# Kernel optimization log

Measured on AMD Instinct MI355X. Metric: run time of the kernel, lower is better.

The kernel has to match this reference:

```python
import jax, jax.numpy as jnp
import numpy as np

NUM_EXPERTS = 32
TOP_K = 4
HIDDEN = 2048
INTER = 768


def setup_inputs() -> dict:
    key = jax.random.key(0)
    k1, k2, k3, k4 = jax.random.split(key, 4)
    hidden_states = jax.random.normal(k1, (4, 512, HIDDEN), dtype=jnp.float32)
    gate = jax.random.normal(k2, (HIDDEN, NUM_EXPERTS), dtype=jnp.float32) * 0.02
    gate_up_proj = jax.random.normal(k3, (NUM_EXPERTS, HIDDEN, 2 * INTER), dtype=jnp.float32) * 0.02
    down_proj = jax.random.normal(k4, (NUM_EXPERTS, INTER, HIDDEN), dtype=jnp.float32) * 0.02
    return {"hidden_states": hidden_states, "gate": gate,
            "gate_up_proj": gate_up_proj, "down_proj": down_proj}


def reference(hidden_states, gate, gate_up_proj, down_proj):
    batch_size = hidden_states.shape[0]
    x = hidden_states.reshape(-1, HIDDEN)  # (T, D)
    num_tokens = x.shape[0]

    # Router
    router_logits = jnp.einsum('TD,DE->TE', x, gate)
    routing_weights = jax.nn.softmax(router_logits.astype(jnp.float32), axis=-1)
    top_k_weights, top_k_indices = jax.lax.top_k(routing_weights, TOP_K)
    top_k_weights = top_k_weights / top_k_weights.sum(axis=-1, keepdims=True)
    top_k_weights = top_k_weights.astype(x.dtype)

    # Scatter top-k weights into full (T, E) matrix
    router_weights = jnp.zeros((num_tokens, NUM_EXPERTS), dtype=x.dtype)
    token_indices = jnp.broadcast_to(jnp.arange(num_tokens)[:, None], top_k_indices.shape)
    router_weights = router_weights.at[token_indices, top_k_indices].set(top_k_weights)

    # Dense all-expert experts pass (faithful to original: computes every expert per token)
    gate_up = jnp.einsum('TD,EDF->TEF', x, gate_up_proj)  # (T, E, 2F)
    g, u = jnp.split(gate_up, 2, axis=-1)
    gated = u * jax.nn.silu(g)  # (T, E, F)
    next_states = jnp.einsum('TEF,EFD->TED', gated, down_proj)
    next_states = (next_states * router_weights[..., None]).sum(axis=1)  # (T, D)
    return next_states.reshape(batch_size, -1, HIDDEN)
```

## Files before the change

kernel.cpp:

```cpp
#include <hip/hip_runtime.h>

#define T_TOKENS 2048
#define HIDDEN   2048
#define NEXPERT  32
#define TOPK     4
#define INTER    768
#define GUF      (2*INTER)
#define NPAIRS   (T_TOKENS*TOPK)
#define BM       128
#define BK       32
#define MT_MAX   95
#define NT1      6
#define NT2      8
#define NK1      (HIDDEN/BK)
#define NK2      (INTER/BK)

typedef short  bh8 __attribute__((ext_vector_type(8)));
typedef float  fx4 __attribute__((ext_vector_type(4)));

#define AS1 __attribute__((address_space(1)))
#define AS3 __attribute__((address_space(3)))

__device__ __forceinline__ void gload_lds16(const void* g, const void* lds_generic){
    __builtin_amdgcn_global_load_lds(
        (const AS1 void*)(unsigned long long)g,
        (AS3 void*)(unsigned int)(unsigned long long)lds_generic,
        16, 0, 0);
}

__device__ __forceinline__ unsigned int pack2bf(float a, float b){
    unsigned ua = __float_as_uint(a) + 0x8000u;
    unsigned ub = __float_as_uint(b) + 0x8000u;
    return __builtin_amdgcn_perm(ub, ua, 0x07060302u);
}
__device__ __forceinline__ unsigned short f2bfu(float f){
    return (unsigned short)((__float_as_uint(f) + 0x8000u) >> 16);
}
__device__ __forceinline__ float bf2f(unsigned short s){
    return __uint_as_float(((unsigned)s)<<16);
}

__global__ void cvt_x_k(const float* __restrict__ x, unsigned short* __restrict__ xb){
    int i = (blockIdx.x*256 + threadIdx.x)*8;
    float4 a = *(const float4*)(x+i);
    float4 b = *(const float4*)(x+i+4);
    uint4 o;
    o.x = pack2bf(a.x,a.y); o.y = pack2bf(a.z,a.w);
    o.z = pack2bf(b.x,b.y); o.w = pack2bf(b.z,b.w);
    *(uint4*)(xb+i) = o;
}

__global__ void router_k(const float* __restrict__ x, const float* __restrict__ gate,
                         int* __restrict__ topk_id, float* __restrict__ topk_w,
                         int* __restrict__ counts){
    const int t = blockIdx.x;
    const int l = threadIdx.x;
    const float* xr = x + (size_t)t*HIDDEN;
    float acc[NEXPERT];
#pragma unroll
    for (int e=0;e<NEXPERT;e++) acc[e]=0.f;
    for (int d=l; d<HIDDEN; d+=64){
        float xv = xr[d];
        const float4* g4 = (const float4*)(gate + (size_t)d*NEXPERT);
#pragma unroll
        for (int i=0;i<8;i++){
            float4 g = g4[i];
            acc[i*4+0] += xv*g.x; acc[i*4+1] += xv*g.y;
            acc[i*4+2] += xv*g.z; acc[i*4+3] += xv*g.w;
        }
    }
#pragma unroll
    for (int e=0;e<NEXPERT;e++){
#pragma unroll
        for (int m=1;m<64;m<<=1) acc[e] += __shfl_xor(acc[e], m, 64);
    }
    int ids[TOPK]; float lv[TOPK];
#pragma unroll
    for (int k=0;k<TOPK;k++){
        float m=-1e30f; int mi=0;
#pragma unroll
        for (int e=0;e<NEXPERT;e++){ if (acc[e]>m){ m=acc[e]; mi=e; } }
        ids[k]=mi; lv[k]=m; acc[mi]=-1e30f;
    }
    float ex[TOPK]; float s=0.f;
#pragma unroll
    for (int k=0;k<TOPK;k++){ ex[k]=__expf(lv[k]-lv[0]); s+=ex[k]; }
    if (l==0){
        float inv = 1.f/s;
#pragma unroll
        for (int k=0;k<TOPK;k++){
            topk_id[t*TOPK+k]=ids[k];
            topk_w[t*TOPK+k]=ex[k]*inv;
            atomicAdd(&counts[ids[k]],1);
        }
    }
}

__global__ void sched_k(const int* __restrict__ counts, int* __restrict__ offs,
                        int* __restrict__ cursors, int* __restrict__ nmt,
                        int* __restrict__ te, int* __restrict__ tr0, int* __restrict__ trn){
    if (threadIdx.x==0 && blockIdx.x==0){
        int tot=0, nm=0;
        for (int e=0;e<NEXPERT;e++){
            int c = counts[e];
            offs[e]=tot; cursors[e]=tot;
            for (int s=0;s<c;s+=BM){
                te[nm]=e; tr0[nm]=tot+s; trn[nm]=(c-s)<BM?(c-s):BM; nm++;
            }
            tot+=c;
        }
        *nmt = nm;
    }
}

__global__ void scatter_k(const int* __restrict__ topk_id, const float* __restrict__ topk_w,
                          int* __restrict__ cursors, int* __restrict__ pair_tok,
                          float* __restrict__ pair_w){
    int g = blockIdx.x*256 + threadIdx.x;
    int e = topk_id[g];
    float w = topk_w[g];
    int pos = atomicAdd(&cursors[e],1);
    pair_tok[pos] = g>>2;
    pair_w[pos]  = w;
}

#define TILE_DECODE()                                              \
    const int nwg = gridDim.x;                                     \
    const int q = nwg>>3, r = nwg&7;                               \
    const int xcd = blockIdx.x & 7, bidx = blockIdx.x >> 3;        \
    const int L = (xcd<r ? xcd*(q+1) : r*(q+1)+(xcd-r)*q) + bidx;  \
    const int mt = L % MT_MAX, nt = L / MT_MAX;                    \
    if (mt >= *nmt) return;                                        \
    const int e = te[mt], row0 = tr0[mt], rows = trn[mt];

__global__ __launch_bounds__(512,4) void gemm1_k(
        const unsigned short* __restrict__ xb, const float* __restrict__ gup,
        const int* __restrict__ nmt, const int* __restrict__ te,
        const int* __restrict__ tr0, const int* __restrict__ trn,
        const int* __restrict__ pair_tok,
        unsigned short* __restrict__ gu){
    __shared__ __align__(16) unsigned short As[2][BM*32];
    __shared__ __align__(16) unsigned short Bs[2][256*40];
    __shared__ int s_tok[BM];

    TILE_DECODE()
    const int n0 = nt*256;

    const int t = threadIdx.x;
    if (t < BM){
        int p = row0 + t; if (p > NPAIRS-1) p = NPAIRS-1;
        s_tok[t] = pair_tok[p];
    }
    __syncthreads();

    const int w = t>>6, lane = t&63;
    const int l15 = lane & 15, kb = lane >> 4;
    const int wr = w & 3, wc = w >> 2;
    const int sA = (l15>>1)&3;

    const int arow = w*16 + (lane>>2);
    const int ck0 = (lane&3) ^ ((lane>>3)&3);
    const unsigned short* asrc = xb + (size_t)s_tok[arow]*HIDDEN + ck0*8;

    const int cp = t & 127, kh = t >> 7;
    const float* bsrc = gup + (size_t)e*HIDDEN*GUF + (size_t)kh*8*GUF + (n0 + 2*cp);
    const unsigned wb0 = (unsigned)((2*cp)*80 + ((kh ^ (cp&3))<<4));

    fx4 acc[2][8];
#pragma unroll
    for (int i=0;i<2;i++)
#pragma unroll
        for (int j=0;j<8;j++) acc[i][j] = (fx4)0.f;

    float2 f0,f1,f2,f3,f4,f5,f6,f7;

#define LOADB1(KS) do{ const float* _bp = bsrc + (size_t)(KS)*BK*GUF;           \
    f0=*(const float2*)(_bp);        f1=*(const float2*)(_bp+GUF);              \
    f2=*(const float2*)(_bp+2*GUF);  f3=*(const float2*)(_bp+3*GUF);            \
    f4=*(const float2*)(_bp+4*GUF);  f5=*(const float2*)(_bp+5*GUF);            \
    f6=*(const float2*)(_bp+6*GUF);  f7=*(const float2*)(_bp+7*GUF); }while(0)

#define WRITEB(BUF) do{ char* _bb = (char*)Bs[BUF];                             \
    uint4 _c0, _c1;                                                             \
    _c0.x=pack2bf(f0.x,f1.x); _c0.y=pack2bf(f2.x,f3.x);                         \
    _c0.z=pack2bf(f4.x,f5.x); _c0.w=pack2bf(f6.x,f7.x);                         \
    _c1.x=pack2bf(f0.y,f1.y); _c1.y=pack2bf(f2.y,f3.y);                         \
    _c1.z=pack2bf(f4.y,f5.y); _c1.w=pack2bf(f6.y,f7.y);                         \
    *(uint4*)(_bb + wb0) = _c0; *(uint4*)(_bb + wb0 + 80) = _c1; }while(0)

#define STAGEA1(KS,BUF) gload_lds16(asrc + (KS)*BK, &As[BUF][(w*16)*32])

#define COMPUTE(BUF) do{                                                        \
    const unsigned short* _Ak = As[BUF];                                        \
    const char* _Bb = (const char*)Bs[BUF];                                     \
    bh8 _a0 = *(const bh8*)(_Ak + (wr*32+l15)*32    + ((kb^sA)<<3));            \
    bh8 _a1 = *(const bh8*)(_Ak + (wr*32+16+l15)*32 + ((kb^sA)<<3));            \
    _Pragma("unroll")                                                           \
    for (int c=0;c<8;c++){                                                      \
        bh8 _b = *(const bh8*)(_Bb + (wc*128 + c*16 + l15)*80 + ((kb^sA)<<4));  \
        acc[0][c] = __builtin_amdgcn_mfma_f32_16x16x32_bf16(_a0,_b,acc[0][c],0,0,0); \
        acc[1][c] = __builtin_amdgcn_mfma_f32_16x16x32_bf16(_a1,_b,acc[1][c],0,0,0); \
    } }while(0)

    STAGEA1(0,0); LOADB1(0);
    __syncthreads();
    WRITEB(0);
    __syncthreads();

    for (int k=0;k<NK1;k++){
        const int kn = k+1;
        if (kn < NK1){ LOADB1(kn); STAGEA1(kn, kn&1); }
        COMPUTE(k&1);
        __syncthreads();
        if (kn < NK1) WRITEB(kn&1);
        __syncthreads();
    }

    const int rbase = wr*32 + kb*4;
#pragma unroll
    for (int mr=0;mr<2;mr++){
#pragma unroll
        for (int qq=0;qq<4;qq++){
            int row = rbase + mr*16 + qq;
            if (row < rows){
                size_t prow = (size_t)(row0 + row)*GUF + n0 + wc*128 + l15;
#pragma unroll
                for (int c=0;c<8;c++)
                    gu[prow + c*16] = f2bfu(acc[mr][c][qq]);
            }
        }
    }
#undef LOADB1
#undef STAGEA1
}

__global__ void silu_k(const unsigned short* __restrict__ gu,
                       const float* __restrict__ pair_w,
                       unsigned short* __restrict__ gated){
    const int t = threadIdx.x;
    const int r = (t >= 96) ? 1 : 0;
    const int jg = t - r*96;
    const int p = blockIdx.x*2 + r;
    bh8 g8 = *(const bh8*)(gu + (size_t)p*GUF + jg*8);
    bh8 u8 = *(const bh8*)(gu + (size_t)p*GUF + INTER + jg*8);
    float wgt = pair_w[p];
    bh8 o;
#pragma unroll
    for (int j=0;j<8;j++){
        float g = bf2f((unsigned short)g8[j]);
        float u = bf2f((unsigned short)u8[j]);
        float sil = g / (1.f + __expf(-g));
        o[j] = (short)f2bfu(sil*u*wgt);
    }
    *(bh8*)(gated + (size_t)p*INTER + jg*8) = o;
}

__global__ __launch_bounds__(512,4) void gemm2_k(
        const unsigned short* __restrict__ gated, const float* __restrict__ down,
        const int* __restrict__ nmt, const int* __restrict__ te,
        const int* __restrict__ tr0, const int* __restrict__ trn,
        const int* __restrict__ pair_tok, float* __restrict__ out){
    __shared__ __align__(16) unsigned short As[2][BM*32];
    __shared__ __align__(16) unsigned short Bs[2][256*40];
    __shared__ int s_tok[BM];

    TILE_DECODE()
    const int n0 = nt*256;

    const int t = threadIdx.x;
    if (t < BM){
        int p = row0 + t; if (p > NPAIRS-1) p = NPAIRS-1;
        s_tok[t] = pair_tok[p];
    }
    __syncthreads();

    const int w = t>>6, lane = t&63;
    const int l15 = lane & 15, kb = lane >> 4;
    const int wr = w & 3, wc = w >> 2;
    const int sA = (l15>>1)&3;

    const int arow = w*16 + (lane>>2);
    const int ck0 = (lane&3) ^ ((lane>>3)&3);
    int ap = row0 + arow; if (ap > NPAIRS-1) ap = NPAIRS-1;
    const unsigned short* asrc = gated + (size_t)ap*INTER + ck0*8;

    const int cp = t & 127, kh = t >> 7;
    const float* bsrc = down + (size_t)e*INTER*HIDDEN + (size_t)kh*8*HIDDEN + (n0 + 2*cp);
    const unsigned wb0 = (unsigned)((2*cp)*80 + ((kh ^ (cp&3))<<4));

    fx4 acc[2][8];
#pragma unroll
    for (int i=0;i<2;i++)
#pragma unroll
        for (int j=0;j<8;j++) acc[i][j] = (fx4)0.f;

    float2 f0,f1,f2,f3,f4,f5,f6,f7;

#define LOADB2(KS) do{ const float* _bp = bsrc + (size_t)(KS)*BK*HIDDEN;        \
    f0=*(const float2*)(_bp);           f1=*(const float2*)(_bp+HIDDEN);        \
    f2=*(const float2*)(_bp+2*HIDDEN);  f3=*(const float2*)(_bp+3*HIDDEN);      \
    f4=*(const float2*)(_bp+4*HIDDEN);  f5=*(const float2*)(_bp+5*HIDDEN);      \
    f6=*(const float2*)(_bp+6*HIDDEN);  f7=*(const float2*)(_bp+7*HIDDEN); }while(0)

#define STAGEA2(KS,BUF) gload_lds16(asrc + (KS)*BK, &As[BUF][(w*16)*32])

    STAGEA2(0,0); LOADB2(0);
    __syncthreads();
    WRITEB(0);
    __syncthreads();

    for (int k=0;k<NK2;k++){
        const int kn = k+1;
        if (kn < NK2){ LOADB2(kn); STAGEA2(kn, kn&1); }
        COMPUTE(k&1);
        __syncthreads();
        if (kn < NK2) WRITEB(kn&1);
        __syncthreads();
    }

    const int rbase = wr*32 + kb*4;
#pragma unroll
    for (int mr=0;mr<2;mr++){
#pragma unroll
        for (int qq=0;qq<4;qq++){
            int row = rbase + mr*16 + qq;
            if (row < rows){
                float* orow = out + (size_t)s_tok[row]*HIDDEN + n0 + wc*128 + l15;
#pragma unroll
                for (int c=0;c<8;c++)
                    atomicAdd(orow + c*16, acc[mr][c][qq]);
            }
        }
    }
}

extern "C" void kernel_launch(void* const* d_in, const int* in_sizes, int n_in,
                              void* d_out, int out_size, void* d_ws, size_t ws_size,
                              hipStream_t stream){
    const float* x    = (const float*)d_in[0];
    const float* gate = (const float*)d_in[1];
    const float* gup  = (const float*)d_in[2];
    const float* down = (const float*)d_in[3];
    float* out = (float*)d_out;
    char*  ws  = (char*)d_ws;

    int*   topk_id  = (int*)  (ws + 0x00000);
    float* topk_w   = (float*)(ws + 0x08000);
    int*   counts   = (int*)  (ws + 0x10000);
    int*   cursors  = (int*)  (ws + 0x10080);
    int*   offs     = (int*)  (ws + 0x10100);
    int*   nmt      = (int*)  (ws + 0x10180);
    int*   te       = (int*)  (ws + 0x10200);
    int*   tr0      = (int*)  (ws + 0x10400);
    int*   trn      = (int*)  (ws + 0x10600);
    int*   pair_tok = (int*)  (ws + 0x10800);
    float* pair_w   = (float*)(ws + 0x18800);
    unsigned short* gated = (unsigned short*)(ws + 0x21000);
    unsigned short* xb    = (unsigned short*)(ws + 0xC60000);
    unsigned short* gu    = (unsigned short*)(ws + 0x1460000);

    hipMemsetAsync(d_out, 0, (size_t)out_size*sizeof(float), stream);
    hipMemsetAsync(counts, 0, NEXPERT*sizeof(int), stream);

    cvt_x_k  <<<T_TOKENS*HIDDEN/(256*8), 256, 0, stream>>>(x, xb);
    router_k <<<T_TOKENS, 64, 0, stream>>>(x, gate, topk_id, topk_w, counts);
    sched_k  <<<1, 64, 0, stream>>>(counts, offs, cursors, nmt, te, tr0, trn);
    scatter_k<<<NPAIRS/256, 256, 0, stream>>>(topk_id, topk_w, cursors, pair_tok, pair_w);
    gemm1_k  <<<MT_MAX*NT1, 512, 0, stream>>>(xb, gup, nmt, te, tr0, trn, pair_tok, gu);
    silu_k   <<<NPAIRS/2, 192, 0, stream>>>(gu, pair_w, gated);
    gemm2_k  <<<MT_MAX*NT2, 512, 0, stream>>>(gated, down, nmt, te, tr0, trn, pair_tok, out);
}
```

Baseline: 510.9 us.

## Enlarge expert GEMM M-tile to 256 rows with 1024-thread blocks

Doubles the row tile of both grouped expert GEMMs from 128 to 256 pairs and uses 1024 threads per block, so each B weight tile (converted from fp32 to bf16 on the fly) is reused across more rows. The B-loading scheme changes to float4 loads with a new swizzled LDS write, each wave computes 64x64 instead of 32x128, and tile decode becomes m-major so adjacent blocks share the same A rows. Larger tiles mean more padding waste for small experts, fewer blocks, and higher register pressure under the launch bounds.

```diff
diff --git a/kernel.cpp b/kernel.cpp
--- a/kernel.cpp
+++ b/kernel.cpp
@@ -7,9 +7,9 @@
 #define INTER    768
 #define GUF      (2*INTER)
 #define NPAIRS   (T_TOKENS*TOPK)
-#define BM       128
+#define BM       256
 #define BK       32
-#define MT_MAX   95
+#define MT_MAX   63
 #define NT1      6
 #define NT2      8
 #define NK1      (HIDDEN/BK)
@@ -124,16 +124,41 @@
     pair_w[pos]  = w;
 }
 
-#define TILE_DECODE()                                              \
+#define TILE_DECODE(NTC)                                           \
     const int nwg = gridDim.x;                                     \
     const int q = nwg>>3, r = nwg&7;                               \
     const int xcd = blockIdx.x & 7, bidx = blockIdx.x >> 3;        \
     const int L = (xcd<r ? xcd*(q+1) : r*(q+1)+(xcd-r)*q) + bidx;  \
-    const int mt = L % MT_MAX, nt = L / MT_MAX;                    \
+    const int mt = L / (NTC), nt = L % (NTC);                      \
     if (mt >= *nmt) return;                                        \
     const int e = te[mt], row0 = tr0[mt], rows = trn[mt];
 
-__global__ __launch_bounds__(512,4) void gemm1_k(
+#define MFMA16(A,B,C) __builtin_amdgcn_mfma_f32_16x16x32_bf16(A,B,C,0,0,0)
+
+#define COMPUTE(BUF) do{                                                        \
+    const unsigned short* _Ak = As[BUF];                                        \
+    const char* _Bb = (const char*)Bs[BUF];                                     \
+    bh8 _a0 = *(const bh8*)(_Ak + (wr*64      + l15)*32 + ((kb^sA)<<3));        \
+    bh8 _a1 = *(const bh8*)(_Ak + (wr*64 + 16 + l15)*32 + ((kb^sA)<<3));        \
+    bh8 _a2 = *(const bh8*)(_Ak + (wr*64 + 32 + l15)*32 + ((kb^sA)<<3));        \
+    bh8 _a3 = *(const bh8*)(_Ak + (wr*64 + 48 + l15)*32 + ((kb^sA)<<3));        \
+    _Pragma("unroll")                                                           \
+    for (int c=0;c<4;c++){                                                      \
+        const int bc = wc*64 + c*16 + l15;                                      \
+        bh8 _b = *(const bh8*)(_Bb + bc*80 + ((kb ^ ((bc>>3)&3))<<4));          \
+        acc[0][c] = MFMA16(_a0,_b,acc[0][c]);                                   \
+        acc[1][c] = MFMA16(_a1,_b,acc[1][c]);                                   \
+        acc[2][c] = MFMA16(_a2,_b,acc[2][c]);                                   \
+        acc[3][c] = MFMA16(_a3,_b,acc[3][c]);                                   \
+    } }while(0)
+
+#define WRITEB(BUF) do{ char* _bb = (char*)Bs[BUF];                             \
+    *(unsigned*)(_bb + wb      ) = pack2bf(rv0.x, rv1.x);                       \
+    *(unsigned*)(_bb + wb +  80) = pack2bf(rv0.y, rv1.y);                       \
+    *(unsigned*)(_bb + wb + 160) = pack2bf(rv0.z, rv1.z);                       \
+    *(unsigned*)(_bb + wb + 240) = pack2bf(rv0.w, rv1.w); }while(0)
+
+__global__ __launch_bounds__(1024,4) void gemm1_k(
         const unsigned short* __restrict__ xb, const float* __restrict__ gup,
         const int* __restrict__ nmt, const int* __restrict__ te,
         const int* __restrict__ tr0, const int* __restrict__ trn,
@@ -143,7 +168,7 @@
     __shared__ __align__(16) unsigned short Bs[2][256*40];
     __shared__ int s_tok[BM];
 
-    TILE_DECODE()
+    TILE_DECODE(NT1)
     const int n0 = nt*256;
 
     const int t = threadIdx.x;
@@ -162,45 +187,22 @@
     const int ck0 = (lane&3) ^ ((lane>>3)&3);
     const unsigned short* asrc = xb + (size_t)s_tok[arow]*HIDDEN + ck0*8;
 
-    const int cp = t & 127, kh = t >> 7;
-    const float* bsrc = gup + (size_t)e*HIDDEN*GUF + (size_t)kh*8*GUF + (n0 + 2*cp);
-    const unsigned wb0 = (unsigned)((2*cp)*80 + ((kh ^ (cp&3))<<4));
-
-    fx4 acc[2][8];
-#pragma unroll
-    for (int i=0;i<2;i++)
-#pragma unroll
-        for (int j=0;j<8;j++) acc[i][j] = (fx4)0.f;
-
-    float2 f0,f1,f2,f3,f4,f5,f6,f7;
-
+    const int tlow = t & 63, th = t >> 6;
+    const int col4 = tlow*4, bd0 = th*2;
+    const int gq = (tlow>>1)&3;
+    const unsigned wb = (unsigned)(col4*80 + (((bd0>>3) ^ gq)<<4) + (bd0&7)*2);
+    const float* bsrc = gup + (size_t)e*HIDDEN*GUF + (size_t)bd0*GUF + (n0 + col4);
+
+    fx4 acc[4][4];
+#pragma unroll
+    for (int i=0;i<4;i++)
+#pragma unroll
+        for (int j=0;j<4;j++) acc[i][j] = (fx4)0.f;
+
+    float4 rv0, rv1;
 #define LOADB1(KS) do{ const float* _bp = bsrc + (size_t)(KS)*BK*GUF;           \
-    f0=*(const float2*)(_bp);        f1=*(const float2*)(_bp+GUF);              \
-    f2=*(const float2*)(_bp+2*GUF);  f3=*(const float2*)(_bp+3*GUF);            \
-    f4=*(const float2*)(_bp+4*GUF);  f5=*(const float2*)(_bp+5*GUF);            \
-    f6=*(const float2*)(_bp+6*GUF);  f7=*(const float2*)(_bp+7*GUF); }while(0)
-
-#define WRITEB(BUF) do{ char* _bb = (char*)Bs[BUF];                             \
-    uint4 _c0, _c1;                                                             \
-    _c0.x=pack2bf(f0.x,f1.x); _c0.y=pack2bf(f2.x,f3.x);                         \
-    _c0.z=pack2bf(f4.x,f5.x); _c0.w=pack2bf(f6.x,f7.x);                         \
-    _c1.x=pack2bf(f0.y,f1.y); _c1.y=pack2bf(f2.y,f3.y);                         \
-    _c1.z=pack2bf(f4.y,f5.y); _c1.w=pack2bf(f6.y,f7.y);                         \
-    *(uint4*)(_bb + wb0) = _c0; *(uint4*)(_bb + wb0 + 80) = _c1; }while(0)
-
+    rv0 = *(const float4*)(_bp); rv1 = *(const float4*)(_bp + GUF); }while(0)
 #define STAGEA1(KS,BUF) gload_lds16(asrc + (KS)*BK, &As[BUF][(w*16)*32])
-
-#define COMPUTE(BUF) do{                                                        \
-    const unsigned short* _Ak = As[BUF];                                        \
-    const char* _Bb = (const char*)Bs[BUF];                                     \
-    bh8 _a0 = *(const bh8*)(_Ak + (wr*32+l15)*32    + ((kb^sA)<<3));            \
-    bh8 _a1 = *(const bh8*)(_Ak + (wr*32+16+l15)*32 + ((kb^sA)<<3));            \
-    _Pragma("unroll")                                                           \
-    for (int c=0;c<8;c++){                                                      \
-        bh8 _b = *(const bh8*)(_Bb + (wc*128 + c*16 + l15)*80 + ((kb^sA)<<4));  \
-        acc[0][c] = __builtin_amdgcn_mfma_f32_16x16x32_bf16(_a0,_b,acc[0][c],0,0,0); \
-        acc[1][c] = __builtin_amdgcn_mfma_f32_16x16x32_bf16(_a1,_b,acc[1][c],0,0,0); \
-    } }while(0)
 
     STAGEA1(0,0); LOADB1(0);
     __syncthreads();
@@ -216,16 +218,15 @@
         __syncthreads();
     }
 
-    const int rbase = wr*32 + kb*4;
-#pragma unroll
-    for (int mr=0;mr<2;mr++){
+#pragma unroll
+    for (int mr=0;mr<4;mr++){
 #pragma unroll
         for (int qq=0;qq<4;qq++){
-            int row = rbase + mr*16 + qq;
+            int row = wr*64 + mr*16 + kb*4 + qq;
             if (row < rows){
-                size_t prow = (size_t)(row0 + row)*GUF + n0 + wc*128 + l15;
-#pragma unroll
-                for (int c=0;c<8;c++)
+                size_t prow = (size_t)(row0 + row)*GUF + n0 + wc*64 + l15;
+#pragma unroll
+                for (int c=0;c<4;c++)
                     gu[prow + c*16] = f2bfu(acc[mr][c][qq]);
             }
         }
@@ -255,7 +256,7 @@
     *(bh8*)(gated + (size_t)p*INTER + jg*8) = o;
 }
 
-__global__ __launch_bounds__(512,4) void gemm2_k(
+__global__ __launch_bounds__(1024,4) void gemm2_k(
         const unsigned short* __restrict__ gated, const float* __restrict__ down,
         const int* __restrict__ nmt, const int* __restrict__ te,
         const int* __restrict__ tr0, const int* __restrict__ trn,
@@ -264,7 +265,7 @@
     __shared__ __align__(16) unsigned short Bs[2][256*40];
     __shared__ int s_tok[BM];
 
-    TILE_DECODE()
+    TILE_DECODE(NT2)
     const int n0 = nt*256;
 
     const int t = threadIdx.x;
@@ -284,24 +285,21 @@
     int ap = row0 + arow; if (ap > NPAIRS-1) ap = NPAIRS-1;
     const unsigned short* asrc = gated + (size_t)ap*INTER + ck0*8;
 
-    const int cp = t & 127, kh = t >> 7;
-    const float* bsrc = down + (size_t)e*INTER*HIDDEN + (size_t)kh*8*HIDDEN + (n0 + 2*cp);
-    const unsigned wb0 = (unsigned)((2*cp)*80 + ((kh ^ (cp&3))<<4));
-
-    fx4 acc[2][8];
-#pragma unroll
-    for (int i=0;i<2;i++)
-#pragma unroll
-        for (int j=0;j<8;j++) acc[i][j] = (fx4)0.f;
-
-    float2 f0,f1,f2,f3,f4,f5,f6,f7;
-
+    const int tlow = t & 63, th = t >> 6;
+    const int col4 = tlow*4, bd0 = th*2;
+    const int gq = (tlow>>1)&3;
+    const unsigned wb = (unsigned)(col4*80 + (((bd0>>3) ^ gq)<<4) + (bd0&7)*2);
+    const float* bsrc = down + (size_t)e*INTER*HIDDEN + (size_t)bd0*HIDDEN + (n0 + col4);
+
+    fx4 acc[4][4];
+#pragma unroll
+    for (int i=0;i<4;i++)
+#pragma unroll
+        for (int j=0;j<4;j++) acc[i][j] = (fx4)0.f;
+
+    float4 rv0, rv1;
 #define LOADB2(KS) do{ const float* _bp = bsrc + (size_t)(KS)*BK*HIDDEN;        \
-    f0=*(const float2*)(_bp);           f1=*(const float2*)(_bp+HIDDEN);        \
-    f2=*(const float2*)(_bp+2*HIDDEN);  f3=*(const float2*)(_bp+3*HIDDEN);      \
-    f4=*(const float2*)(_bp+4*HIDDEN);  f5=*(const float2*)(_bp+5*HIDDEN);      \
-    f6=*(const float2*)(_bp+6*HIDDEN);  f7=*(const float2*)(_bp+7*HIDDEN); }while(0)
-
+    rv0 = *(const float4*)(_bp); rv1 = *(const float4*)(_bp + HIDDEN); }while(0)
 #define STAGEA2(KS,BUF) gload_lds16(asrc + (KS)*BK, &As[BUF][(w*16)*32])
 
     STAGEA2(0,0); LOADB2(0);
@@ -318,20 +316,21 @@
         __syncthreads();
     }
 
-    const int rbase = wr*32 + kb*4;
-#pragma unroll
-    for (int mr=0;mr<2;mr++){
+#pragma unroll
+    for (int mr=0;mr<4;mr++){
 #pragma unroll
         for (int qq=0;qq<4;qq++){
-            int row = rbase + mr*16 + qq;
+            int row = wr*64 + mr*16 + kb*4 + qq;
             if (row < rows){
-                float* orow = out + (size_t)s_tok[row]*HIDDEN + n0 + wc*128 + l15;
-#pragma unroll
-                for (int c=0;c<8;c++)
+                float* orow = out + (size_t)s_tok[row]*HIDDEN + n0 + wc*64 + l15;
+#pragma unroll
+                for (int c=0;c<4;c++)
                     atomicAdd(orow + c*16, acc[mr][c][qq]);
             }
         }
     }
+#undef LOADB2
+#undef STAGEA2
 }
 
 extern "C" void kernel_launch(void* const* d_in, const int* in_sizes, int n_in,
@@ -366,7 +365,7 @@
     router_k <<<T_TOKENS, 64, 0, stream>>>(x, gate, topk_id, topk_w, counts);
     sched_k  <<<1, 64, 0, stream>>>(counts, offs, cursors, nmt, te, tr0, trn);
     scatter_k<<<NPAIRS/256, 256, 0, stream>>>(topk_id, topk_w, cursors, pair_tok, pair_w);
-    gemm1_k  <<<MT_MAX*NT1, 512, 0, stream>>>(xb, gup, nmt, te, tr0, trn, pair_tok, gu);
+    gemm1_k  <<<MT_MAX*NT1, 1024, 0, stream>>>(xb, gup, nmt, te, tr0, trn, pair_tok, gu);
     silu_k   <<<NPAIRS/2, 192, 0, stream>>>(gu, pair_w, gated);
-    gemm2_k  <<<MT_MAX*NT2, 512, 0, stream>>>(gated, down, nmt, te, tr0, trn, pair_tok, out);
-}
+    gemm2_k  <<<MT_MAX*NT2, 1024, 0, stream>>>(gated, down, nmt, te, tr0, trn, pair_tok, out);
+}
```

New measurement: 490.2 us. -4.1%, faster.
